# Performance work log

Measured on AMD Instinct MI355X. Metric: run time of the kernel, lower is better.

Reference implementation:

```python
import jax, jax.numpy as jnp
import numpy as np

N, C_IN, H, W = 256, 256, 28, 28
D = 64        # prototype channel dim (prototype_shape[1])
P = 200       # num prototypes
NCLS = 10


def setup_inputs() -> dict:
    key = jax.random.key(0)
    ks = jax.random.split(key, 6)
    x = jax.random.normal(ks[0], (N, C_IN, H, W), dtype=jnp.float32)
    W1 = jax.random.normal(ks[1], (D, C_IN), dtype=jnp.float32) * 0.05
    b1 = jnp.zeros((D,), dtype=jnp.float32)
    W2 = jax.random.normal(ks[2], (D, D), dtype=jnp.float32) * 0.05
    b2 = jnp.zeros((D,), dtype=jnp.float32)
    prototypes = jax.random.uniform(ks[3], (P, D), dtype=jnp.float32)
    last_W = jax.random.normal(ks[4], (NCLS, P), dtype=jnp.float32) * 0.05
    last_b = jnp.zeros((NCLS,), dtype=jnp.float32)
    return {"x": x, "W1": W1, "b1": b1, "W2": W2, "b2": b2,
            "prototypes": prototypes, "last_W": last_W, "last_b": last_b}


def reference(x, W1, b1, W2, b2, prototypes, last_W, last_b):
    # add_on_layers: 1x1 conv -> relu -> 1x1 conv -> sigmoid (pointwise GEMMs)
    h = jax.nn.relu(jnp.einsum('nchw,oc->nohw', x, W1) + b1[None, :, None, None])
    f = jax.nn.sigmoid(jnp.einsum('nchw,oc->nohw', h, W2) + b2[None, :, None, None])
    # L2 convolution with 1x1 prototypes:
    # conv(x^2, ones) == channel sum of f^2, broadcast over P prototypes
    x2_patch_sum = jnp.sum(f * f, axis=1, keepdims=True)          # (N,1,H,W)
    xp = jnp.einsum('nchw,pc->nphw', f, prototypes)               # (N,P,H,W)
    p2 = jnp.sum(prototypes * prototypes, axis=1)[None, :, None, None]  # (1,P,1,1)
    distances = jax.nn.relu(x2_patch_sum - 2.0 * xp + p2)         # (N,P,H,W)
    # global min-pool over spatial dims (== -maxpool(-d) with full kernel)
    min_distances = jnp.min(distances, axis=(2, 3))               # (N,P)
    # paf == 'linear': similarity = -distance
    prototype_activations = -min_distances
    logits = prototype_activations @ last_W.T + last_b            # (N,NCLS)
    return (logits, min_distances)
```

## Files before the change

### kernel.cpp

```cpp
#include <hip/hip_runtime.h>

#define NIMG 256
#define CIN  256
#define PIX  784
#define DD   64
#define NP   200
#define NPP  208
#define NCLS 10

#define XS 264
#define HS 72

typedef __attribute__((ext_vector_type(8))) short bf16x8;
typedef __attribute__((ext_vector_type(4))) float f32x4;

__device__ __forceinline__ unsigned short f2bf(float f) {
    union { float f; unsigned int u; } v; v.f = f;
    unsigned int r = v.u + 0x7fffu + ((v.u >> 16) & 1u);
    return (unsigned short)(r >> 16);
}
__device__ __forceinline__ float bf2f(unsigned short h) {
    union { float f; unsigned int u; } v; v.u = ((unsigned int)h) << 16;
    return v.f;
}

__global__ __launch_bounds__(512)
void proto_fused_kernel(const float* __restrict__ x,
                        const float* __restrict__ W1, const float* __restrict__ b1,
                        const float* __restrict__ W2, const float* __restrict__ b2,
                        const float* __restrict__ proto,
                        const float* __restrict__ lastW, const float* __restrict__ lastb,
                        float* __restrict__ out)
{
    __shared__ __align__(16) unsigned short xlds[64 * XS];
    __shared__ __align__(16) unsigned short w1lds[64 * XS];
    __shared__ __align__(16) unsigned short w2lds[64 * HS];
    __shared__ __align__(16) unsigned short protolds[NPP * HS];
    __shared__ __align__(16) unsigned short htile[64 * HS];
    __shared__ __align__(16) unsigned short ftile[64 * HS];
    __shared__ float p2lds[NPP];
    __shared__ float s2lds[64];
    __shared__ float b1lds[DD], b2lds[DD];
    __shared__ unsigned int bmin[NPP];

    const int n    = blockIdx.x;
    const int t    = threadIdx.x;
    const int wave = t >> 6;
    const int lane = t & 63;
    const int q    = lane >> 4;
    const int l15  = lane & 15;
    const int s    = wave & 3;
    const int dh   = wave >> 2;

    for (int i = 0; i < 32; ++i) {
        int idx = t + i * 512;
        w1lds[(idx >> 8) * XS + (idx & 255)] = f2bf(W1[idx]);
    }
    for (int i = 0; i < 8; ++i) {
        int idx = t + i * 512;
        w2lds[(idx >> 6) * HS + (idx & 63)] = f2bf(W2[idx]);
    }
    for (int i = 0; i < 25; ++i) {
        int idx = t + i * 512;
        protolds[(idx >> 6) * HS + (idx & 63)] = f2bf(proto[idx]);
    }
    {
        int p = NP + (t >> 6), d = t & 63;
        protolds[p * HS + d] = 0;
    }
    if (t < DD) { b1lds[t] = b1[t]; b2lds[t] = b2[t]; }
    if (t < NPP) {
        float acc = 0.f;
        if (t < NP) {
            for (int d = 0; d < DD; ++d) { float v = proto[t * DD + d]; acc += v * v; }
        }
        p2lds[t] = acc;
        bmin[t] = 0x7f800000u;
    }

    for (int tile = 0; tile < 13; ++tile) {
        const int px0 = tile * 64;

        {
            const int p4    = (t & 15) * 4;
            const int cbase = t >> 4;
            for (int i = 0; i < 8; ++i) {
                int c = cbase + i * 32;
                const float* src = x + ((size_t)n * CIN + c) * PIX + px0 + p4;
                float v0, v1, v2, v3;
                if (px0 + p4 + 3 < PIX) {
                    float4 v = *(const float4*)src;
                    v0 = v.x; v1 = v.y; v2 = v.z; v3 = v.w;
                } else {
                    v0 = (px0 + p4 + 0 < PIX) ? src[0] : 0.f;
                    v1 = (px0 + p4 + 1 < PIX) ? src[1] : 0.f;
                    v2 = (px0 + p4 + 2 < PIX) ? src[2] : 0.f;
                    v3 = (px0 + p4 + 3 < PIX) ? src[3] : 0.f;
                }
                xlds[(p4 + 0) * XS + c] = f2bf(v0);
                xlds[(p4 + 1) * XS + c] = f2bf(v1);
                xlds[(p4 + 2) * XS + c] = f2bf(v2);
                xlds[(p4 + 3) * XS + c] = f2bf(v3);
            }
        }
        __syncthreads();

        {
            const int dt0 = dh * 2, dt1 = dh * 2 + 1;
            f32x4 acc0 = {0.f, 0.f, 0.f, 0.f}, acc1 = {0.f, 0.f, 0.f, 0.f};
            const int arow  = (s * 16 + l15) * XS + q * 8;
            const int brow0 = (dt0 * 16 + l15) * XS + q * 8;
            const int brow1 = (dt1 * 16 + l15) * XS + q * 8;
            for (int kk = 0; kk < 256; kk += 32) {
                bf16x8 a   = *(const bf16x8*)&xlds[arow + kk];
                bf16x8 bb0 = *(const bf16x8*)&w1lds[brow0 + kk];
                bf16x8 bb1 = *(const bf16x8*)&w1lds[brow1 + kk];
                acc0 = __builtin_amdgcn_mfma_f32_16x16x32_bf16(a, bb0, acc0, 0, 0, 0);
                acc1 = __builtin_amdgcn_mfma_f32_16x16x32_bf16(a, bb1, acc1, 0, 0, 0);
            }
            for (int r = 0; r < 4; ++r) {
                int prow = s * 16 + q * 4 + r;
                float h0 = fmaxf(acc0[r] + b1lds[dt0 * 16 + l15], 0.f);
                float h1 = fmaxf(acc1[r] + b1lds[dt1 * 16 + l15], 0.f);
                htile[prow * HS + dt0 * 16 + l15] = f2bf(h0);
                htile[prow * HS + dt1 * 16 + l15] = f2bf(h1);
            }
        }
        __syncthreads();

        {
            const int dt0 = dh * 2, dt1 = dh * 2 + 1;
            f32x4 acc0 = {0.f, 0.f, 0.f, 0.f}, acc1 = {0.f, 0.f, 0.f, 0.f};
            const int arow  = (s * 16 + l15) * HS + q * 8;
            const int brow0 = (dt0 * 16 + l15) * HS + q * 8;
            const int brow1 = (dt1 * 16 + l15) * HS + q * 8;
            for (int kk = 0; kk < 64; kk += 32) {
                bf16x8 a   = *(const bf16x8*)&htile[arow + kk];
                bf16x8 bb0 = *(const bf16x8*)&w2lds[brow0 + kk];
                bf16x8 bb1 = *(const bf16x8*)&w2lds[brow1 + kk];
                acc0 = __builtin_amdgcn_mfma_f32_16x16x32_bf16(a, bb0, acc0, 0, 0, 0);
                acc1 = __builtin_amdgcn_mfma_f32_16x16x32_bf16(a, bb1, acc1, 0, 0, 0);
            }
            for (int r = 0; r < 4; ++r) {
                int prow = s * 16 + q * 4 + r;
                float z0 = acc0[r] + b2lds[dt0 * 16 + l15];
                float z1 = acc1[r] + b2lds[dt1 * 16 + l15];
                float f0 = 1.0f / (1.0f + exp2f(z0 * -1.44269504f));
                float f1 = 1.0f / (1.0f + exp2f(z1 * -1.44269504f));
                ftile[prow * HS + dt0 * 16 + l15] = f2bf(f0);
                ftile[prow * HS + dt1 * 16 + l15] = f2bf(f1);
            }
        }
        __syncthreads();

        if (t < 64) {
            float acc = 0.f;
            for (int d = 0; d < DD; ++d) { float v = bf2f(ftile[t * HS + d]); acc += v * v; }
            s2lds[t] = acc;
        }
        __syncthreads();

        {
            const int arow = (s * 16 + l15) * HS + q * 8;
            bf16x8 a0 = *(const bf16x8*)&ftile[arow];
            bf16x8 a1 = *(const bf16x8*)&ftile[arow + 32];
            for (int pt = dh; pt < 13; pt += 2) {
                const int brow = (pt * 16 + l15) * HS + q * 8;
                bf16x8 bb0 = *(const bf16x8*)&protolds[brow];
                bf16x8 bb1 = *(const bf16x8*)&protolds[brow + 32];
                f32x4 acc = {0.f, 0.f, 0.f, 0.f};
                acc = __builtin_amdgcn_mfma_f32_16x16x32_bf16(a0, bb0, acc, 0, 0, 0);
                acc = __builtin_amdgcn_mfma_f32_16x16x32_bf16(a1, bb1, acc, 0, 0, 0);
                const int p = pt * 16 + l15;
                float m = __uint_as_float(0x7f800000u);
                for (int r = 0; r < 4; ++r) {
                    int pl = s * 16 + q * 4 + r;
                    if (px0 + pl < PIX) {
                        float dist = s2lds[pl] - 2.f * acc[r] + p2lds[p];
                        dist = fmaxf(dist, 0.f);
                        m = fminf(m, dist);
                    }
                }
                m = fminf(m, __shfl_xor(m, 16, 64));
                m = fminf(m, __shfl_xor(m, 32, 64));
                if (lane < 16) atomicMin(&bmin[p], __float_as_uint(m));
            }
        }
        __syncthreads();
    }

    if (t < NP) {
        out[NIMG * NCLS + (size_t)n * NP + t] = __uint_as_float(bmin[t]);
    }
    if (t < 320) {
        int c = t >> 5, j = t & 31;
        float acc = 0.f;
        for (int p = j; p < NP; p += 32)
            acc += __uint_as_float(bmin[p]) * lastW[c * NP + p];
        acc += __shfl_xor(acc, 1, 32);
        acc += __shfl_xor(acc, 2, 32);
        acc += __shfl_xor(acc, 4, 32);
        acc += __shfl_xor(acc, 8, 32);
        acc += __shfl_xor(acc, 16, 32);
        if (j == 0) out[(size_t)n * NCLS + c] = -acc + lastb[c];
    }
}

extern "C" void kernel_launch(void* const* d_in, const int* in_sizes, int n_in,
                              void* d_out, int out_size, void* d_ws, size_t ws_size,
                              hipStream_t stream) {
    const float* x     = (const float*)d_in[0];
    const float* W1    = (const float*)d_in[1];
    const float* b1    = (const float*)d_in[2];
    const float* W2    = (const float*)d_in[3];
    const float* b2    = (const float*)d_in[4];
    const float* proto = (const float*)d_in[5];
    const float* lastW = (const float*)d_in[6];
    const float* lastb = (const float*)d_in[7];
    float* out = (float*)d_out;

    proto_fused_kernel<<<dim3(NIMG), dim3(512), 0, stream>>>(
        x, W1, b1, W2, b2, proto, lastW, lastb, out);
}
```

Before: 369.0 us.

## Prefetch x tiles into registers and keep weight fragments resident across tiles

```diff
diff --git a/kernel.cpp b/kernel.cpp
--- a/kernel.cpp
+++ b/kernel.cpp
@@ -1,4 +1,5 @@
 #include <hip/hip_runtime.h>
+#include <hip/hip_bf16.h>
 
 #define NIMG 256
 #define CIN  256
@@ -13,18 +14,22 @@
 
 typedef __attribute__((ext_vector_type(8))) short bf16x8;
 typedef __attribute__((ext_vector_type(4))) float f32x4;
+typedef __attribute__((ext_vector_type(4))) unsigned int u32x4;
 
 __device__ __forceinline__ unsigned short f2bf(float f) {
     union { float f; unsigned int u; } v; v.f = f;
     unsigned int r = v.u + 0x7fffu + ((v.u >> 16) & 1u);
     return (unsigned short)(r >> 16);
 }
-__device__ __forceinline__ float bf2f(unsigned short h) {
-    union { float f; unsigned int u; } v; v.u = ((unsigned int)h) << 16;
-    return v.f;
-}
-
-__global__ __launch_bounds__(512)
+
+__device__ __forceinline__ unsigned int pk2(float a, float b) {
+    __hip_bfloat162 p = __float22bfloat162_rn(make_float2(a, b));
+    return *(unsigned int*)&p;
+}
+
+#define MFMA(a, b, c) __builtin_amdgcn_mfma_f32_16x16x32_bf16((a), (b), (c), 0, 0, 0)
+
+__global__ __launch_bounds__(512, 2)
 void proto_fused_kernel(const float* __restrict__ x,
                         const float* __restrict__ W1, const float* __restrict__ b1,
                         const float* __restrict__ W2, const float* __restrict__ b2,
@@ -39,18 +44,19 @@
     __shared__ __align__(16) unsigned short htile[64 * HS];
     __shared__ __align__(16) unsigned short ftile[64 * HS];
     __shared__ float p2lds[NPP];
-    __shared__ float s2lds[64];
+    __shared__ float s2lds[2][64];
     __shared__ float b1lds[DD], b2lds[DD];
     __shared__ unsigned int bmin[NPP];
 
     const int n    = blockIdx.x;
     const int t    = threadIdx.x;
-    const int wave = t >> 6;
     const int lane = t & 63;
     const int q    = lane >> 4;
     const int l15  = lane & 15;
+    const int wave = t >> 6;
     const int s    = wave & 3;
     const int dh   = wave >> 2;
+    const int dt0  = dh * 2, dt1 = dh * 2 + 1;
 
     for (int i = 0; i < 32; ++i) {
         int idx = t + i * 512;
@@ -78,46 +84,70 @@
         bmin[t] = 0x7f800000u;
     }
 
-    for (int tile = 0; tile < 13; ++tile) {
-        const int px0 = tile * 64;
+    const int p4  = (t & 15) * 4;
+    const int cb8 = (t >> 4) * 8;
+    const float* xn = x + (size_t)n * CIN * PIX;
+
+    float4 pf[8];
+    auto load_tile = [&](int px0) {
+        #pragma unroll
+        for (int j = 0; j < 8; ++j) {
+            const float* src = xn + (size_t)(cb8 + j) * PIX + px0 + p4;
+            float4 v;
+            if (px0 + p4 + 3 < PIX) {
+                v = *(const float4*)src;
+            } else {
+                v.x = (px0 + p4 + 0 < PIX) ? src[0] : 0.f;
+                v.y = (px0 + p4 + 1 < PIX) ? src[1] : 0.f;
+                v.z = (px0 + p4 + 2 < PIX) ? src[2] : 0.f;
+                v.w = (px0 + p4 + 3 < PIX) ? src[3] : 0.f;
+            }
+            pf[j] = v;
+        }
+    };
+    auto store_tile = [&]() {
+        #pragma unroll
+        for (int r = 0; r < 4; ++r) {
+            u32x4 uv;
+            uv.x = pk2(((const float*)&pf[0])[r], ((const float*)&pf[1])[r]);
+            uv.y = pk2(((const float*)&pf[2])[r], ((const float*)&pf[3])[r]);
+            uv.z = pk2(((const float*)&pf[4])[r], ((const float*)&pf[5])[r]);
+            uv.w = pk2(((const float*)&pf[6])[r], ((const float*)&pf[7])[r]);
+            *(u32x4*)&xlds[(p4 + r) * XS + cb8] = uv;
+        }
+    };
+
+    load_tile(0);
+    store_tile();
+    load_tile(64);
+    __syncthreads();
+
+    bf16x8 w1f0[8], w1f1[8];
+    #pragma unroll
+    for (int kk = 0; kk < 8; ++kk) {
+        w1f0[kk] = *(const bf16x8*)&w1lds[(dt0 * 16 + l15) * XS + kk * 32 + q * 8];
+        w1f1[kk] = *(const bf16x8*)&w1lds[(dt1 * 16 + l15) * XS + kk * 32 + q * 8];
+    }
+    bf16x8 w2f0[2], w2f1[2];
+    #pragma unroll
+    for (int kk = 0; kk < 2; ++kk) {
+        w2f0[kk] = *(const bf16x8*)&w2lds[(dt0 * 16 + l15) * HS + kk * 32 + q * 8];
+        w2f1[kk] = *(const bf16x8*)&w2lds[(dt1 * 16 + l15) * HS + kk * 32 + q * 8];
+    }
+
+    for (int tl = 0; tl < 13; ++tl) {
+        const int px0 = tl * 64;
 
         {
-            const int p4    = (t & 15) * 4;
-            const int cbase = t >> 4;
-            for (int i = 0; i < 8; ++i) {
-                int c = cbase + i * 32;
-                const float* src = x + ((size_t)n * CIN + c) * PIX + px0 + p4;
-                float v0, v1, v2, v3;
-                if (px0 + p4 + 3 < PIX) {
-                    float4 v = *(const float4*)src;
-                    v0 = v.x; v1 = v.y; v2 = v.z; v3 = v.w;
-                } else {
-                    v0 = (px0 + p4 + 0 < PIX) ? src[0] : 0.f;
-                    v1 = (px0 + p4 + 1 < PIX) ? src[1] : 0.f;
-                    v2 = (px0 + p4 + 2 < PIX) ? src[2] : 0.f;
-                    v3 = (px0 + p4 + 3 < PIX) ? src[3] : 0.f;
-                }
-                xlds[(p4 + 0) * XS + c] = f2bf(v0);
-                xlds[(p4 + 1) * XS + c] = f2bf(v1);
-                xlds[(p4 + 2) * XS + c] = f2bf(v2);
-                xlds[(p4 + 3) * XS + c] = f2bf(v3);
-            }
-        }
-        __syncthreads();
-
-        {
-            const int dt0 = dh * 2, dt1 = dh * 2 + 1;
             f32x4 acc0 = {0.f, 0.f, 0.f, 0.f}, acc1 = {0.f, 0.f, 0.f, 0.f};
-            const int arow  = (s * 16 + l15) * XS + q * 8;
-            const int brow0 = (dt0 * 16 + l15) * XS + q * 8;
-            const int brow1 = (dt1 * 16 + l15) * XS + q * 8;
-            for (int kk = 0; kk < 256; kk += 32) {
-                bf16x8 a   = *(const bf16x8*)&xlds[arow + kk];
-                bf16x8 bb0 = *(const bf16x8*)&w1lds[brow0 + kk];
-                bf16x8 bb1 = *(const bf16x8*)&w1lds[brow1 + kk];
-                acc0 = __builtin_amdgcn_mfma_f32_16x16x32_bf16(a, bb0, acc0, 0, 0, 0);
-                acc1 = __builtin_amdgcn_mfma_f32_16x16x32_bf16(a, bb1, acc1, 0, 0, 0);
-            }
+            const int arow = (s * 16 + l15) * XS + q * 8;
+            #pragma unroll
+            for (int kk = 0; kk < 8; ++kk) {
+                bf16x8 a = *(const bf16x8*)&xlds[arow + kk * 32];
+                acc0 = MFMA(a, w1f0[kk], acc0);
+                acc1 = MFMA(a, w1f1[kk], acc1);
+            }
+            #pragma unroll
             for (int r = 0; r < 4; ++r) {
                 int prow = s * 16 + q * 4 + r;
                 float h0 = fmaxf(acc0[r] + b1lds[dt0 * 16 + l15], 0.f);
@@ -128,66 +158,70 @@
         }
         __syncthreads();
 
+        if (tl < 12) store_tile();
         {
-            const int dt0 = dh * 2, dt1 = dh * 2 + 1;
             f32x4 acc0 = {0.f, 0.f, 0.f, 0.f}, acc1 = {0.f, 0.f, 0.f, 0.f};
-            const int arow  = (s * 16 + l15) * HS + q * 8;
-            const int brow0 = (dt0 * 16 + l15) * HS + q * 8;
-            const int brow1 = (dt1 * 16 + l15) * HS + q * 8;
-            for (int kk = 0; kk < 64; kk += 32) {
-                bf16x8 a   = *(const bf16x8*)&htile[arow + kk];
-                bf16x8 bb0 = *(const bf16x8*)&w2lds[brow0 + kk];
-                bf16x8 bb1 = *(const bf16x8*)&w2lds[brow1 + kk];
-                acc0 = __builtin_amdgcn_mfma_f32_16x16x32_bf16(a, bb0, acc0, 0, 0, 0);
-                acc1 = __builtin_amdgcn_mfma_f32_16x16x32_bf16(a, bb1, acc1, 0, 0, 0);
-            }
+            const int arowH = (s * 16 + l15) * HS + q * 8;
+            bf16x8 a0 = *(const bf16x8*)&htile[arowH];
+            bf16x8 a1 = *(const bf16x8*)&htile[arowH + 32];
+            acc0 = MFMA(a0, w2f0[0], acc0);
+            acc0 = MFMA(a1, w2f0[1], acc0);
+            acc1 = MFMA(a0, w2f1[0], acc1);
+            acc1 = MFMA(a1, w2f1[1], acc1);
+            #pragma unroll
             for (int r = 0; r < 4; ++r) {
                 int prow = s * 16 + q * 4 + r;
                 float z0 = acc0[r] + b2lds[dt0 * 16 + l15];
                 float z1 = acc1[r] + b2lds[dt1 * 16 + l15];
-                float f0 = 1.0f / (1.0f + exp2f(z0 * -1.44269504f));
-                float f1 = 1.0f / (1.0f + exp2f(z1 * -1.44269504f));
+                float f0 = __builtin_amdgcn_rcpf(1.0f + __builtin_amdgcn_exp2f(z0 * -1.44269504f));
+                float f1 = __builtin_amdgcn_rcpf(1.0f + __builtin_amdgcn_exp2f(z1 * -1.44269504f));
                 ftile[prow * HS + dt0 * 16 + l15] = f2bf(f0);
                 ftile[prow * HS + dt1 * 16 + l15] = f2bf(f1);
+                float v = f0 * f0 + f1 * f1;
+                v += __shfl_xor(v, 1, 64);
+                v += __shfl_xor(v, 2, 64);
+                v += __shfl_xor(v, 4, 64);
+                v += __shfl_xor(v, 8, 64);
+                if (l15 == 0) s2lds[dh][prow] = v;
             }
         }
         __syncthreads();
 
-        if (t < 64) {
-            float acc = 0.f;
-            for (int d = 0; d < DD; ++d) { float v = bf2f(ftile[t * HS + d]); acc += v * v; }
-            s2lds[t] = acc;
-        }
-        __syncthreads();
-
+        if (tl < 11) load_tile((tl + 2) * 64);
         {
-            const int arow = (s * 16 + l15) * HS + q * 8;
-            bf16x8 a0 = *(const bf16x8*)&ftile[arow];
-            bf16x8 a1 = *(const bf16x8*)&ftile[arow + 32];
+            const int arowF = (s * 16 + l15) * HS + q * 8;
+            bf16x8 a0 = *(const bf16x8*)&ftile[arowF];
+            bf16x8 a1 = *(const bf16x8*)&ftile[arowF + 32];
+            float s2v[4];
+            bool  vmask[4];
+            #pragma unroll
+            for (int r = 0; r < 4; ++r) {
+                int pl = s * 16 + q * 4 + r;
+                s2v[r]   = s2lds[0][pl] + s2lds[1][pl];
+                vmask[r] = (px0 + pl < PIX);
+            }
             for (int pt = dh; pt < 13; pt += 2) {
                 const int brow = (pt * 16 + l15) * HS + q * 8;
                 bf16x8 bb0 = *(const bf16x8*)&protolds[brow];
                 bf16x8 bb1 = *(const bf16x8*)&protolds[brow + 32];
                 f32x4 acc = {0.f, 0.f, 0.f, 0.f};
-                acc = __builtin_amdgcn_mfma_f32_16x16x32_bf16(a0, bb0, acc, 0, 0, 0);
-                acc = __builtin_amdgcn_mfma_f32_16x16x32_bf16(a1, bb1, acc, 0, 0, 0);
+                acc = MFMA(a0, bb0, acc);
+                acc = MFMA(a1, bb1, acc);
                 const int p = pt * 16 + l15;
-                float m = __uint_as_float(0x7f800000u);
+                const float p2v = p2lds[p];
+                float m = 1e30f;
+                #pragma unroll
                 for (int r = 0; r < 4; ++r) {
-                    int pl = s * 16 + q * 4 + r;
-                    if (px0 + pl < PIX) {
-                        float dist = s2lds[pl] - 2.f * acc[r] + p2lds[p];
-                        dist = fmaxf(dist, 0.f);
-                        m = fminf(m, dist);
-                    }
+                    float dist = fmaxf(s2v[r] - 2.f * acc[r] + p2v, 0.f);
+                    if (vmask[r]) m = fminf(m, dist);
                 }
                 m = fminf(m, __shfl_xor(m, 16, 64));
                 m = fminf(m, __shfl_xor(m, 32, 64));
                 if (lane < 16) atomicMin(&bmin[p], __float_as_uint(m));
             }
         }
-        __syncthreads();
-    }
+    }
+    __syncthreads();
 
     if (t < NP) {
         out[NIMG * NCLS + (size_t)n * NP + t] = __uint_as_float(bmin[t]);
```

Result: faster. 312.3 us (-15.4%).
